# Kernel optimization log

Hardware: AMD Instinct MI355X
Metric: run time of the kernel (lower is better)

Reference implementation:

```python
import jax, jax.numpy as jnp
import numpy as np

# env_params constants (chosen, see shape_source)
ETN, EAN = 64, 64          # entity type / attribute nums
RTN, RAN = 128, 64         # relationship type / attribute nums
ME, MR = 2048, 65536       # max entities / relationships
TES, THM, HID = 16, 256, 128
ENV = ETN + RTN + TES      # 208 = GRU input size


def _lin(key, out_d, in_d):
    k1, k2 = jax.random.split(key)
    lim = 1.0 / np.sqrt(in_d)
    W = jax.random.uniform(k1, (out_d, in_d), minval=-lim, maxval=lim, dtype=jnp.float32)
    b = jax.random.uniform(k2, (out_d,), minval=-lim, maxval=lim, dtype=jnp.float32)
    return W, b


def setup_inputs() -> dict:
    key = jax.random.key(0)
    ks = jax.random.split(key, 32)
    # entity: one-hot type in cols [0:ETN], random attributes after
    etype = jax.nn.one_hot(jax.random.randint(ks[0], (ME,), 0, ETN), ETN, dtype=jnp.float32)
    entity = jnp.concatenate([etype, jax.random.normal(ks[1], (ME, EAN), jnp.float32)], axis=1)
    rtype = jax.nn.one_hot(jax.random.randint(ks[2], (MR,), 0, RTN), RTN, dtype=jnp.float32)
    relationship = jnp.concatenate([rtype, jax.random.normal(ks[3], (MR, RAN + ME), jnp.float32)], axis=1)
    target = jax.random.normal(ks[4], (ME + EAN + MR + RAN,), jnp.float32)
    action_mask = (jax.random.uniform(ks[5], (THM,)) > 0.2).astype(jnp.float32)
    # entity encoder: 128 -> 32 -> 8 -> 1
    ew1, eb1 = _lin(ks[6], 32, ETN + EAN)
    ew2, eb2 = _lin(ks[7], 8, 32)
    ew3, eb3 = _lin(ks[8], 1, 8)
    # relationship encoder: 2240 -> 128 -> 64 -> 32 -> 8 -> 1
    rin = RTN + RAN + ME
    rw1, rb1 = _lin(ks[9], 128, rin)
    rw2, rb2 = _lin(ks[10], 64, 128)
    rw3, rb3 = _lin(ks[11], 32, 64)
    rw4, rb4 = _lin(ks[12], 8, 32)
    rw5, rb5 = _lin(ks[13], 1, 8)
    # target encoder: 67712 -> 64 -> 16
    tin = ME + EAN + MR + RAN
    tw1, tb1 = _lin(ks[14], 64, tin)
    tw2, tb2 = _lin(ks[15], TES, 64)
    # GRUCell(208, 128)
    lim = 1.0 / np.sqrt(HID)
    wih = jax.random.uniform(ks[16], (3 * HID, ENV), minval=-lim, maxval=lim, dtype=jnp.float32)
    whh = jax.random.uniform(ks[17], (3 * HID, HID), minval=-lim, maxval=lim, dtype=jnp.float32)
    bih = jax.random.uniform(ks[18], (3 * HID,), minval=-lim, maxval=lim, dtype=jnp.float32)
    bhh = jax.random.uniform(ks[19], (3 * HID,), minval=-lim, maxval=lim, dtype=jnp.float32)
    hidden = jax.random.normal(ks[20], (1, HID), jnp.float32)
    aw, ab = _lin(ks[21], THM, HID)
    return dict(entity=entity, relationship=relationship, target=target, action_mask=action_mask,
                ew1=ew1, eb1=eb1, ew2=ew2, eb2=eb2, ew3=ew3, eb3=eb3,
                rw1=rw1, rb1=rb1, rw2=rw2, rb2=rb2, rw3=rw3, rb3=rb3, rw4=rw4, rb4=rb4, rw5=rw5, rb5=rb5,
                tw1=tw1, tb1=tb1, tw2=tw2, tb2=tb2,
                wih=wih, whh=whh, bih=bih, bhh=bhh, hidden=hidden, aw=aw, ab=ab)


def _masked_group_max(onehot_mask, feat):
    # onehot_mask: [N, T] (==1 where row belongs to type t); feat: [N, 1]
    m = onehot_mask == 1.0
    vals = jnp.max(jnp.where(m, feat, -jnp.inf), axis=0)      # [T]
    return jnp.where(jnp.any(m, axis=0), vals, 0.0)            # empty group -> 0


def reference(entity, relationship, target, action_mask,
              ew1, eb1, ew2, eb2, ew3, eb3,
              rw1, rb1, rw2, rb2, rw3, rb3, rw4, rb4, rw5, rb5,
              tw1, tb1, tw2, tb2,
              wih, whh, bih, bhh, hidden, aw, ab):
    relu = jax.nn.relu
    # entity encoder -> [ME, 1]
    ef = relu(entity @ ew1.T + eb1)
    ef = relu(ef @ ew2.T + eb2)
    ef = ef @ ew3.T + eb3
    # relationship encoder -> [MR, 1]
    rf = relu(relationship @ rw1.T + rb1)
    rf = relu(rf @ rw2.T + rb2)
    rf = relu(rf @ rw3.T + rb3)
    rf = relu(rf @ rw4.T + rb4)
    rf = rf @ rw5.T + rb5
    # one-hot masked segment max over type columns
    eg = _masked_group_max(entity[:, :ETN], ef)          # [ETN]
    rg = _masked_group_max(relationship[:, :RTN], rf)    # [RTN]
    # target encoder -> [TES]
    tf = relu(target @ tw1.T + tb1) @ tw2.T + tb2
    env = jnp.concatenate([eg, rg, tf]).reshape(1, ENV)
    # GRUCell (torch gate order: r, z, n)
    gx = env @ wih.T + bih
    gh = hidden @ whh.T + bhh
    xr, xz, xn = jnp.split(gx, 3, axis=1)
    hr, hz, hn = jnp.split(gh, 3, axis=1)
    r = jax.nn.sigmoid(xr + hr)
    z = jax.nn.sigmoid(xz + hz)
    n = jnp.tanh(xn + r * hn)
    h = ((1.0 - z) * n + z * hidden).reshape(-1)         # [128]
    logits = jax.nn.softmax(h @ aw.T + ab, axis=0)       # [THM]
    return logits * action_mask
```

## Files before the change

### kernel.cpp

```cpp
#include <hip/hip_runtime.h>
#include <stdint.h>

typedef unsigned short u16;
typedef short s16x8 __attribute__((ext_vector_type(8)));
typedef float f32x4 __attribute__((ext_vector_type(4)));

__device__ __forceinline__ float bf2f(u16 u) {
  union { unsigned u; float f; } c; c.u = ((unsigned)u) << 16; return c.f;
}
__device__ __forceinline__ u16 f2bf(float f) {
  union { float f; unsigned u; } c; c.f = f;
  unsigned r = c.u + 0x7FFFu + ((c.u >> 16) & 1u);
  return (u16)(r >> 16);
}
__device__ __forceinline__ unsigned encf(float x) {
  union { float f; unsigned u; } c; c.f = x;
  return (c.u & 0x80000000u) ? ~c.u : (c.u | 0x80000000u);
}
__device__ __forceinline__ float decf(unsigned e) {
  union { unsigned u; float f; } c;
  c.u = (e & 0x80000000u) ? (e ^ 0x80000000u) : ~e;
  return c.f;
}
__device__ __forceinline__ f32x4 mfma16(s16x8 a, s16x8 b, f32x4 c) {
  return __builtin_amdgcn_mfma_f32_16x16x32_bf16(a, b, c, 0, 0, 0);
}
__device__ __forceinline__ float relu(float x) { return x > 0.f ? x : 0.f; }

template <int F32>
__device__ __forceinline__ void loadf8(const void* p, size_t ei, float* o) {
  if (F32) {
    const float* f = (const float*)p + ei;
    f32x4 a = *(const f32x4*)f;
    f32x4 b = *(const f32x4*)(f + 4);
#pragma unroll
    for (int j = 0; j < 4; ++j) { o[j] = a[j]; o[4 + j] = b[j]; }
  } else {
    s16x8 v = *(const s16x8*)((const u16*)p + ei);
#pragma unroll
    for (int j = 0; j < 8; ++j) o[j] = bf2f((u16)v[j]);
  }
}
template <int F32>
__device__ __forceinline__ s16x8 load8b(const void* p, size_t ei) {
  if (F32) {
    float o[8]; loadf8<1>(p, ei, o);
    s16x8 r;
#pragma unroll
    for (int j = 0; j < 8; ++j) r[j] = (short)f2bf(o[j]);
    return r;
  } else {
    return *(const s16x8*)((const u16*)p + ei);
  }
}
template <int F32>
__device__ __forceinline__ float ld1(const void* p, size_t ei) {
  return F32 ? ((const float*)p)[ei] : bf2f(((const u16*)p)[ei]);
}

__global__ void k_detect(const u16* __restrict__ entity, const u16* __restrict__ rel,
                         unsigned* __restrict__ ws) {
  __shared__ unsigned cnt[256];
  const int t = threadIdx.x;
  ws[t] = 0u;
  unsigned c = 0;
  for (int i = t; i < 16384; i += 256) {
    unsigned u = rel[i];
    if ((u & 0x7F80u) == 0x7F80u) ++c;
  }
  for (int i = t; i < 8192; i += 256) {
    unsigned u = entity[i];
    if ((u & 0x7F80u) == 0x7F80u) ++c;
  }
  cnt[t] = c;
  __syncthreads();
  for (int st = 128; st > 0; st >>= 1) {
    if (t < st) cnt[t] += cnt[t + st];
    __syncthreads();
  }
  if (t == 0) ws[256] = cnt[0] ? 1u : 0u;
}

template <int F32>
__global__ __launch_bounds__(256) void k_ent(
    const void* __restrict__ entity, const void* __restrict__ ew1, const void* __restrict__ eb1,
    const void* __restrict__ ew2, const void* __restrict__ eb2,
    const void* __restrict__ ew3, const void* __restrict__ eb3,
    unsigned* __restrict__ egws, const unsigned* __restrict__ flag) {
  if (*flag != (unsigned)F32) return;
  __shared__ __align__(16) u16 xl[32 * 136];
  __shared__ __align__(16) u16 w1l[32 * 136];
  __shared__ float h1l[32 * 33];
  __shared__ float h2l[32 * 9];
  const int t = threadIdx.x;
  const int row0 = blockIdx.x * 32;
#pragma unroll
  for (int p = 0; p < 2; ++p) {
    int lin = p * 256 + t, rr = lin >> 4, cc = lin & 15;
    *(s16x8*)(xl + rr * 136 + cc * 8) =
        load8b<F32>(entity, (size_t)(row0 + rr) * 128 + cc * 8);
    *(s16x8*)(w1l + rr * 136 + cc * 8) = load8b<F32>(ew1, (size_t)rr * 128 + cc * 8);
  }
  __syncthreads();
  {
    const int r = t >> 3, g = t & 7;
    float acc[4] = {0.f, 0.f, 0.f, 0.f};
#pragma unroll 4
    for (int c = 0; c < 16; ++c) {
      s16x8 xv = *(const s16x8*)(xl + r * 136 + c * 8);
      float xf[8];
#pragma unroll
      for (int j = 0; j < 8; ++j) xf[j] = bf2f((u16)xv[j]);
#pragma unroll
      for (int s = 0; s < 4; ++s) {
        s16x8 wv = *(const s16x8*)(w1l + (g + 8 * s) * 136 + c * 8);
#pragma unroll
        for (int j = 0; j < 8; ++j) acc[s] += xf[j] * bf2f((u16)wv[j]);
      }
    }
#pragma unroll
    for (int s = 0; s < 4; ++s)
      h1l[r * 33 + g + 8 * s] = relu(acc[s] + ld1<F32>(eb1, g + 8 * s));
  }
  __syncthreads();
  {
    const int r = t >> 3, o = t & 7;
    float a = ld1<F32>(eb2, o);
#pragma unroll 8
    for (int k = 0; k < 32; ++k) a += h1l[r * 33 + k] * ld1<F32>(ew2, o * 32 + k);
    h2l[r * 9 + o] = relu(a);
  }
  __syncthreads();
  if (t < 32) {
    float s = ld1<F32>(eb3, 0);
#pragma unroll
    for (int k = 0; k < 8; ++k) s += h2l[t * 9 + k] * ld1<F32>(ew3, k);
    int ty = 0;
#pragma unroll
    for (int c = 0; c < 8; ++c) {
      s16x8 v = *(const s16x8*)(xl + t * 136 + c * 8);
#pragma unroll
      for (int j = 0; j < 8; ++j)
        if ((u16)v[j] == (u16)0x3F80) ty = c * 8 + j;
    }
    atomicMax(egws + ty, encf(s));
  }
}

template <int F32>
__global__ __launch_bounds__(256) void k_tgt(const void* __restrict__ target,
                                             const void* __restrict__ tw1,
                                             float* __restrict__ tpart,
                                             const unsigned* __restrict__ flag) {
  if (*flag != (unsigned)F32) return;
  __shared__ float red[256];
  const int t = threadIdx.x;
  const int o = blockIdx.x >> 2, c = blockIdx.x & 3;
  float a = 0.f;
  for (int i = t; i < 2116; i += 256) {
    float xf[8], wf[8];
    loadf8<F32>(target, (size_t)c * 16928 + i * 8, xf);
    loadf8<F32>(tw1, (size_t)o * 67712 + c * 16928 + i * 8, wf);
#pragma unroll
    for (int j = 0; j < 8; ++j) a += xf[j] * wf[j];
  }
  red[t] = a;
  __syncthreads();
  for (int st = 128; st > 0; st >>= 1) {
    if (t < st) red[t] += red[t + st];
    __syncthreads();
  }
  if (t == 0) atomicAdd(tpart + o, red[0]);
}

#define RK 2240
template <int F32>
__global__ __launch_bounds__(256) void k_rel(
    const void* __restrict__ rel, const void* __restrict__ rw1, const void* __restrict__ rb1,
    const void* __restrict__ rw2, const void* __restrict__ rb2,
    const void* __restrict__ rw3, const void* __restrict__ rb3,
    const void* __restrict__ rw4, const void* __restrict__ rb4,
    const void* __restrict__ rw5, const void* __restrict__ rb5,
    unsigned* __restrict__ rgws, const unsigned* __restrict__ flag) {
  if (*flag != (unsigned)F32) return;
  __shared__ __align__(16) unsigned char sm[53760];
  u16* smA = (u16*)sm;
  u16* smB = (u16*)(sm + 8192);
  u16* r0 = (u16*)sm;
  u16* smRF = (u16*)(sm + 18432);
  int* styp = (int*)(sm + 53248);

  const int t = threadIdx.x;
  const int lane = t & 63;
  const int wid = t >> 6;
  const int row0 = blockIdx.x * 128;
  const int fr = lane & 15, fq = lane >> 4;

  if (t < 128) {
    int ty = 0;
#pragma unroll 4
    for (int c = 0; c < 16; ++c) {
      s16x8 v = load8b<F32>(rel, (size_t)(row0 + t) * RK + c * 8);
#pragma unroll
      for (int j = 0; j < 8; ++j)
        if ((u16)v[j] == (u16)0x3F80) ty = c * 8 + j;
    }
    styp[t] = ty;
  }

  const int wm = wid >> 1, wn = wid & 1;
  f32x4 acc[4][4];
#pragma unroll
  for (int i = 0; i < 4; ++i)
#pragma unroll
    for (int j = 0; j < 4; ++j) acc[i][j] = f32x4{0.f, 0.f, 0.f, 0.f};

  const size_t gA0 = (size_t)(row0 + (t >> 2)) * RK + (t & 3) * 8;
  const size_t gB0 = (size_t)(t >> 2) * RK + (t & 3) * 8;

  for (int ki = 0; ki < 70; ++ki) {
    const int k0 = ki * 32;
    s16x8 va0 = load8b<F32>(rel, gA0 + k0);
    s16x8 va1 = load8b<F32>(rel, gA0 + (size_t)64 * RK + k0);
    s16x8 vb0 = load8b<F32>(rw1, gB0 + k0);
    s16x8 vb1 = load8b<F32>(rw1, gB0 + (size_t)64 * RK + k0);
    __syncthreads();
    *(s16x8*)(smA + t * 8) = va0;
    *(s16x8*)(smA + 2048 + t * 8) = va1;
    *(s16x8*)(smB + t * 8) = vb0;
    *(s16x8*)(smB + 2048 + t * 8) = vb1;
    __syncthreads();
    s16x8 a[4], b[4];
#pragma unroll
    for (int i = 0; i < 4; ++i)
      a[i] = *(const s16x8*)(smA + (wm * 64 + i * 16 + fr) * 32 + fq * 8);
#pragma unroll
    for (int j = 0; j < 4; ++j)
      b[j] = *(const s16x8*)(smB + (wn * 64 + j * 16 + fr) * 32 + fq * 8);
#pragma unroll
    for (int i = 0; i < 4; ++i)
#pragma unroll
      for (int j = 0; j < 4; ++j) acc[i][j] = mfma16(a[i], b[j], acc[i][j]);
  }
  __syncthreads();

#pragma unroll
  for (int j = 0; j < 4; ++j) {
    const int col = wn * 64 + j * 16 + fr;
    const float bias = ld1<F32>(rb1, col);
#pragma unroll
    for (int i = 0; i < 4; ++i) {
      const int rbase = wm * 64 + i * 16 + fq * 4;
#pragma unroll
      for (int r = 0; r < 4; ++r)
        smRF[(rbase + r) * 136 + col] = f2bf(relu(acc[i][j][r] + bias));
    }
  }
  __syncthreads();

  if (t < 128) {
    const u16* rfrow = smRF + t * 136;
    for (int o = 0; o < 64; ++o) {
      float a = ld1<F32>(rb2, o);
      for (int k = 0; k < 128; k += 8) {
        float wf[8];
        loadf8<F32>(rw2, o * 128 + k, wf);
#pragma unroll
        for (int j = 0; j < 8; ++j) a += bf2f(rfrow[k + j]) * wf[j];
      }
      r0[t * 72 + o] = f2bf(relu(a));
    }
    const u16* h2row = r0 + t * 72;
    float h3[32];
#pragma unroll
    for (int o = 0; o < 32; ++o) {
      float a = ld1<F32>(rb3, o);
      for (int k = 0; k < 64; k += 8) {
        float wf[8];
        loadf8<F32>(rw3, o * 64 + k, wf);
#pragma unroll
        for (int j = 0; j < 8; ++j) a += bf2f(h2row[k + j]) * wf[j];
      }
      h3[o] = relu(a);
    }
    float h4[8];
#pragma unroll
    for (int o = 0; o < 8; ++o) {
      float a = ld1<F32>(rb4, o);
#pragma unroll
      for (int k = 0; k < 32; ++k) a += h3[k] * ld1<F32>(rw4, o * 32 + k);
      h4[o] = relu(a);
    }
    float s = ld1<F32>(rb5, 0);
#pragma unroll
    for (int k = 0; k < 8; ++k) s += h4[k] * ld1<F32>(rw5, k);
    atomicMax(rgws + styp[t], encf(s));
  }
}

template <int F32>
__global__ __launch_bounds__(256) void k_fin(
    const unsigned* __restrict__ egws, const unsigned* __restrict__ rgws,
    const float* __restrict__ tpart, const void* __restrict__ tb1,
    const void* __restrict__ tw2, const void* __restrict__ tb2,
    const void* __restrict__ wih, const void* __restrict__ whh,
    const void* __restrict__ bih, const void* __restrict__ bhh,
    const void* __restrict__ hidden, const void* __restrict__ aw,
    const void* __restrict__ ab, const void* __restrict__ amask,
    void* __restrict__ outp, const unsigned* __restrict__ flag) {
  if (*flag != (unsigned)F32) return;
  __shared__ float env[208];
  __shared__ float th1[64];
  __shared__ float gx[384], gh[384];
  __shared__ float hv[128], hid[128];
  __shared__ float red[256];
  const int t = threadIdx.x;
  if (t < 64) {
    unsigned e = egws[t];
    env[t] = e ? decf(e) : 0.f;
    th1[t] = relu(tpart[t] + ld1<F32>(tb1, t));
  }
  if (t >= 64 && t < 192) {
    unsigned e = rgws[t - 64];
    env[t] = e ? decf(e) : 0.f;
  }
  if (t < 128) hid[t] = ld1<F32>(hidden, t);
  __syncthreads();
  if (t < 16) {
    float a = ld1<F32>(tb2, t);
    for (int k = 0; k < 64; k += 8) {
      float wf[8];
      loadf8<F32>(tw2, t * 64 + k, wf);
#pragma unroll
      for (int j = 0; j < 8; ++j) a += th1[k + j] * wf[j];
    }
    env[192 + t] = a;
  }
  __syncthreads();
  for (int o = t; o < 384; o += 256) {
    float ax = ld1<F32>(bih, o);
#pragma unroll 2
    for (int c = 0; c < 26; ++c) {
      float wf[8];
      loadf8<F32>(wih, (size_t)o * 208 + c * 8, wf);
#pragma unroll
      for (int j = 0; j < 8; ++j) ax += env[c * 8 + j] * wf[j];
    }
    gx[o] = ax;
    float ah = ld1<F32>(bhh, o);
#pragma unroll 2
    for (int c = 0; c < 16; ++c) {
      float wf[8];
      loadf8<F32>(whh, (size_t)o * 128 + c * 8, wf);
#pragma unroll
      for (int j = 0; j < 8; ++j) ah += hid[c * 8 + j] * wf[j];
    }
    gh[o] = ah;
  }
  __syncthreads();
  if (t < 128) {
    float r = 1.f / (1.f + expf(-(gx[t] + gh[t])));
    float z = 1.f / (1.f + expf(-(gx[128 + t] + gh[128 + t])));
    float n = tanhf(gx[256 + t] + r * gh[256 + t]);
    hv[t] = (1.f - z) * n + z * hid[t];
  }
  __syncthreads();
  float s = ld1<F32>(ab, t);
#pragma unroll 4
  for (int c = 0; c < 16; ++c) {
    float wf[8];
    loadf8<F32>(aw, (size_t)t * 128 + c * 8, wf);
#pragma unroll
    for (int j = 0; j < 8; ++j) s += hv[c * 8 + j] * wf[j];
  }
  red[t] = s;
  __syncthreads();
  for (int st = 128; st > 0; st >>= 1) {
    if (t < st) red[t] = fmaxf(red[t], red[t + st]);
    __syncthreads();
  }
  float m = red[0];
  __syncthreads();
  float e = expf(s - m);
  red[t] = e;
  __syncthreads();
  for (int st = 128; st > 0; st >>= 1) {
    if (t < st) red[t] += red[t + st];
    __syncthreads();
  }
  float v = e * (1.f / red[0]) * ld1<F32>(amask, t);
  if (F32) ((float*)outp)[t] = v;
  else ((u16*)outp)[t] = f2bf(v);
}

extern "C" void kernel_launch(void* const* d_in, const int* in_sizes, int n_in,
                              void* d_out, int out_size, void* d_ws, size_t ws_size,
                              hipStream_t stream) {
  const void* entity = d_in[0];
  const void* rel    = d_in[1];
  const void* target = d_in[2];
  const void* amask  = d_in[3];
  const void* ew1 = d_in[4];  const void* eb1 = d_in[5];
  const void* ew2 = d_in[6];  const void* eb2 = d_in[7];
  const void* ew3 = d_in[8];  const void* eb3 = d_in[9];
  const void* rw1 = d_in[10]; const void* rb1 = d_in[11];
  const void* rw2 = d_in[12]; const void* rb2 = d_in[13];
  const void* rw3 = d_in[14]; const void* rb3 = d_in[15];
  const void* rw4 = d_in[16]; const void* rb4 = d_in[17];
  const void* rw5 = d_in[18]; const void* rb5 = d_in[19];
  const void* tw1 = d_in[20]; const void* tb1 = d_in[21];
  const void* tw2 = d_in[22]; const void* tb2 = d_in[23];
  const void* wih = d_in[24]; const void* whh = d_in[25];
  const void* bih = d_in[26]; const void* bhh = d_in[27];
  const void* hidden = d_in[28];
  const void* aw = d_in[29];  const void* ab = d_in[30];

  unsigned* ws = (unsigned*)d_ws;
  unsigned* egws = ws;
  unsigned* rgws = ws + 64;
  float* tpart = (float*)(ws + 192);
  const unsigned* flag = ws + 256;

  hipLaunchKernelGGL(k_detect, dim3(1), dim3(256), 0, stream,
                     (const u16*)entity, (const u16*)rel, ws);

  hipLaunchKernelGGL((k_ent<0>), dim3(64), dim3(256), 0, stream,
                     entity, ew1, eb1, ew2, eb2, ew3, eb3, egws, flag);
  hipLaunchKernelGGL((k_ent<1>), dim3(64), dim3(256), 0, stream,
                     entity, ew1, eb1, ew2, eb2, ew3, eb3, egws, flag);

  hipLaunchKernelGGL((k_tgt<0>), dim3(256), dim3(256), 0, stream, target, tw1, tpart, flag);
  hipLaunchKernelGGL((k_tgt<1>), dim3(256), dim3(256), 0, stream, target, tw1, tpart, flag);

  hipLaunchKernelGGL((k_rel<0>), dim3(512), dim3(256), 0, stream,
                     rel, rw1, rb1, rw2, rb2, rw3, rb3, rw4, rb4, rw5, rb5, rgws, flag);
  hipLaunchKernelGGL((k_rel<1>), dim3(512), dim3(256), 0, stream,
                     rel, rw1, rb1, rw2, rb2, rw3, rb3, rw4, rb4, rw5, rb5, rgws, flag);

  hipLaunchKernelGGL((k_fin<0>), dim3(1), dim3(256), 0, stream,
                     egws, rgws, tpart, tb1, tw2, tb2, wih, whh, bih, bhh,
                     hidden, aw, ab, amask, d_out, flag);
  hipLaunchKernelGGL((k_fin<1>), dim3(1), dim3(256), 0, stream,
                     egws, rgws, tpart, tb1, tw2, tb2, wih, whh, bih, bhh,
                     hidden, aw, ab, amask, d_out, flag);
}
```

Measured before the change: 1.090 ms.

## Add bf16 relationship encoder kernel with async global-to-LDS double buffering

Replaces the bf16 path of the relationship encoder with a new kernel. It streams relationship rows and the first-layer weights straight into swizzled LDS using global_load_lds, double-buffered across K steps. The first two layers run on MFMA from shared memory, and the type index is found from the one-hot columns during the first K tiles. The aim is to hide global load latency and avoid register staging in the 2240-wide first layer. The cost is a large LDS footprint (about 69 KB per block), which caps occupancy.

```diff
diff --git a/kernel.cpp b/kernel.cpp
--- a/kernel.cpp
+++ b/kernel.cpp
@@ -26,6 +26,14 @@
   return __builtin_amdgcn_mfma_f32_16x16x32_bf16(a, b, c, 0, 0, 0);
 }
 __device__ __forceinline__ float relu(float x) { return x > 0.f ? x : 0.f; }
+
+__device__ __forceinline__ void gload_lds16(const void* g, void* l) {
+  auto* gp = reinterpret_cast<const __attribute__((address_space(1))) unsigned*>(
+      reinterpret_cast<uintptr_t>(g));
+  auto* lp = reinterpret_cast<__attribute__((address_space(3))) unsigned*>(
+      reinterpret_cast<uintptr_t>(l));
+  __builtin_amdgcn_global_load_lds(gp, lp, 16, 0, 0);
+}
 
 template <int F32>
 __device__ __forceinline__ void loadf8(const void* p, size_t ei, float* o) {
@@ -296,6 +304,187 @@
     for (int k = 0; k < 8; ++k) s += h4[k] * ld1<F32>(rw5, k);
     atomicMax(rgws + styp[t], encf(s));
   }
+}
+
+__global__ __launch_bounds__(256, 2) void k_relb(
+    const u16* __restrict__ rel, const u16* __restrict__ rw1, const u16* __restrict__ rb1,
+    const u16* __restrict__ rw2, const u16* __restrict__ rb2,
+    const u16* __restrict__ rw3, const u16* __restrict__ rb3,
+    const u16* __restrict__ rw4, const u16* __restrict__ rb4,
+    const u16* __restrict__ rw5, const u16* __restrict__ rb5,
+    unsigned* __restrict__ rgws, const unsigned* __restrict__ flag) {
+  if (*flag != 0u) return;
+  __shared__ __align__(16) unsigned char sm[70656];
+  const int t = threadIdx.x;
+  const int lane = t & 63;
+  const int wid = t >> 6;
+  const int fr = lane & 15, fq = lane >> 4;
+  const int wm = wid >> 1, wn = wid & 1;
+  const int l8 = lane >> 3;
+  const int row0 = blockIdx.x * 128;
+  const int swu = ((lane & 7) ^ l8) * 8;
+  const int swa = (fr & 7) << 3;
+
+  f32x4 acc[4][4];
+#pragma unroll
+  for (int i = 0; i < 4; ++i)
+#pragma unroll
+    for (int j = 0; j < 4; ++j) acc[i][j] = f32x4{0.f, 0.f, 0.f, 0.f};
+
+  {
+    unsigned char* ba = sm;
+    unsigned char* bb = sm + 16384;
+#pragma unroll
+    for (int it = 0; it < 4; ++it) {
+      const int rr = wid * 32 + it * 8;
+      gload_lds16(rel + (size_t)(row0 + rr + l8) * RK + swu, ba + rr * 128);
+      gload_lds16(rw1 + (size_t)(rr + l8) * RK + swu, bb + rr * 128);
+    }
+  }
+  __syncthreads();
+
+  int ty = 0;
+#pragma unroll 1
+  for (int ki = 0; ki < 35; ++ki) {
+    if (ki < 34) {
+      unsigned char* ba = sm + ((ki + 1) & 1) * 32768;
+      unsigned char* bb = ba + 16384;
+      const int k0 = (ki + 1) * 64;
+#pragma unroll
+      for (int it = 0; it < 4; ++it) {
+        const int rr = wid * 32 + it * 8;
+        gload_lds16(rel + (size_t)(row0 + rr + l8) * RK + k0 + swu, ba + rr * 128);
+        gload_lds16(rw1 + (size_t)(rr + l8) * RK + k0 + swu, bb + rr * 128);
+      }
+    }
+    const u16* ba = (const u16*)(sm + (ki & 1) * 32768);
+    const u16* bb = ba + 8192;
+#pragma unroll
+    for (int ks = 0; ks < 2; ++ks) {
+      s16x8 a[4], b[4];
+#pragma unroll
+      for (int i = 0; i < 4; ++i)
+        a[i] = *(const s16x8*)(ba + (wm * 64 + i * 16 + fr) * 64 + ((ks * 32 + fq * 8) ^ swa));
+#pragma unroll
+      for (int j = 0; j < 4; ++j)
+        b[j] = *(const s16x8*)(bb + (wn * 64 + j * 16 + fr) * 64 + ((ks * 32 + fq * 8) ^ swa));
+#pragma unroll
+      for (int i = 0; i < 4; ++i)
+#pragma unroll
+        for (int j = 0; j < 4; ++j) acc[i][j] = mfma16(a[i], b[j], acc[i][j]);
+    }
+    if (ki < 2) {
+      const int r = t >> 1, hs = t & 1;
+      const int rsw = (r & 7) << 3;
+#pragma unroll
+      for (int c = 0; c < 4; ++c) {
+        const int cc = hs * 4 + c;
+        s16x8 v = *(const s16x8*)(ba + r * 64 + ((cc * 8) ^ rsw));
+#pragma unroll
+        for (int j = 0; j < 8; ++j)
+          if ((u16)v[j] == (u16)0x3F80) ty = ki * 64 + cc * 8 + j;
+      }
+    }
+    __syncthreads();
+  }
+
+  u16* smRF = (u16*)sm;
+  u16* w2l = (u16*)(sm + 34816);
+  u16* h2 = (u16*)(sm + 52224);
+#pragma unroll
+  for (int j = 0; j < 4; ++j) {
+    const int col = wn * 64 + j * 16 + fr;
+    const float bias = bf2f(rb1[col]);
+#pragma unroll
+    for (int i = 0; i < 4; ++i) {
+      const int rbase = wm * 64 + i * 16 + fq * 4;
+#pragma unroll
+      for (int r = 0; r < 4; ++r)
+        smRF[(rbase + r) * 136 + col] = f2bf(relu(acc[i][j][r] + bias));
+    }
+  }
+  for (int q = t; q < 1024; q += 256) {
+    const int rr = q >> 4, cc = q & 15;
+    *(s16x8*)(w2l + rr * 136 + cc * 8) = *(const s16x8*)(rw2 + rr * 128 + cc * 8);
+  }
+  __syncthreads();
+
+  f32x4 c2[4][2];
+#pragma unroll
+  for (int i = 0; i < 4; ++i)
+#pragma unroll
+    for (int j = 0; j < 2; ++j) c2[i][j] = f32x4{0.f, 0.f, 0.f, 0.f};
+#pragma unroll
+  for (int ks = 0; ks < 4; ++ks) {
+    s16x8 a2[4], b2[2];
+#pragma unroll
+    for (int i = 0; i < 4; ++i)
+      a2[i] = *(const s16x8*)(smRF + (wm * 64 + i * 16 + fr) * 136 + ks * 32 + fq * 8);
+#pragma unroll
+    for (int j = 0; j < 2; ++j)
+      b2[j] = *(const s16x8*)(w2l + (wn * 32 + j * 16 + fr) * 136 + ks * 32 + fq * 8);
+#pragma unroll
+    for (int i = 0; i < 4; ++i)
+#pragma unroll
+      for (int j = 0; j < 2; ++j) c2[i][j] = mfma16(a2[i], b2[j], c2[i][j]);
+  }
+#pragma unroll
+  for (int j = 0; j < 2; ++j) {
+    const int col = wn * 32 + j * 16 + fr;
+    const float b2v = bf2f(rb2[col]);
+#pragma unroll
+    for (int i = 0; i < 4; ++i) {
+      const int rbase = wm * 64 + i * 16 + fq * 4;
+#pragma unroll
+      for (int r = 0; r < 4; ++r)
+        h2[(rbase + r) * 72 + col] = f2bf(relu(c2[i][j][r] + b2v));
+    }
+  }
+  __syncthreads();
+
+  const int r3 = t >> 1, hs = t & 1;
+  const u16* h2row = h2 + r3 * 72;
+  float h3a[16];
+#pragma unroll
+  for (int o = 0; o < 16; ++o) h3a[o] = bf2f(rb3[hs * 16 + o]);
+#pragma unroll 2
+  for (int kc = 0; kc < 8; ++kc) {
+    s16x8 hv = *(const s16x8*)(h2row + kc * 8);
+    float hf[8];
+#pragma unroll
+    for (int j = 0; j < 8; ++j) hf[j] = bf2f((u16)hv[j]);
+#pragma unroll
+    for (int o = 0; o < 16; ++o) {
+      s16x8 wv = *(const s16x8*)(rw3 + (size_t)(hs * 16 + o) * 64 + kc * 8);
+#pragma unroll
+      for (int j = 0; j < 8; ++j) h3a[o] += hf[j] * bf2f((u16)wv[j]);
+    }
+  }
+  float vo[16], vp[16];
+#pragma unroll
+  for (int o = 0; o < 16; ++o) {
+    vo[o] = relu(h3a[o]);
+    vp[o] = __shfl_xor(vo[o], 1);
+  }
+  float h4[4];
+#pragma unroll
+  for (int oo = 0; oo < 4; ++oo) {
+    const int o = hs * 4 + oo;
+    float s1 = 0.f, s2 = 0.f;
+#pragma unroll
+    for (int k = 0; k < 16; ++k) {
+      s1 += vo[k] * bf2f(rw4[o * 32 + hs * 16 + k]);
+      s2 += vp[k] * bf2f(rw4[o * 32 + (1 - hs) * 16 + k]);
+    }
+    h4[oo] = relu(s1 + s2 + bf2f(rb4[o]));
+  }
+  float sp = 0.f;
+#pragma unroll
+  for (int oo = 0; oo < 4; ++oo) sp += h4[oo] * bf2f(rw5[hs * 4 + oo]);
+  const float sfull = sp + __shfl_xor(sp, 1) + bf2f(rb5[0]);
+  const int tp2 = __shfl_xor(ty, 1);
+  const int tmax = ty > tp2 ? ty : tp2;
+  if (hs == 0) atomicMax(rgws + tmax, encf(sfull));
 }
 
 template <int F32>
@@ -432,8 +621,11 @@
   hipLaunchKernelGGL((k_tgt<0>), dim3(256), dim3(256), 0, stream, target, tw1, tpart, flag);
   hipLaunchKernelGGL((k_tgt<1>), dim3(256), dim3(256), 0, stream, target, tw1, tpart, flag);
 
-  hipLaunchKernelGGL((k_rel<0>), dim3(512), dim3(256), 0, stream,
-                     rel, rw1, rb1, rw2, rb2, rw3, rb3, rw4, rb4, rw5, rb5, rgws, flag);
+  hipLaunchKernelGGL(k_relb, dim3(512), dim3(256), 0, stream,
+                     (const u16*)rel, (const u16*)rw1, (const u16*)rb1,
+                     (const u16*)rw2, (const u16*)rb2, (const u16*)rw3,
+                     (const u16*)rb3, (const u16*)rw4, (const u16*)rb4,
+                     (const u16*)rw5, (const u16*)rb5, rgws, flag);
   hipLaunchKernelGGL((k_rel<1>), dim3(512), dim3(256), 0, stream,
                      rel, rw1, rb1, rw2, rb2, rw3, rb3, rw4, rb4, rw5, rb5, rgws, flag);
 
```

Result: no change. 1.086 ms (-0.4%).

## Add fp32-specialized relationship encoder kernel loading MFMA fragments from global memory

Applied to the files above, without the earlier changes.

Adds a dedicated fp32 path for the relationship encoder. It reads the fp32 rows and rw1 weights straight from global memory into registers, converts them to bf16 in registers and feeds MFMA, with no shared-memory staging of the first layer's operands. The row type is found by scanning for the one-hot column first. The goal is to cut shared-memory traffic and synchronisation in the dominant 65536x2240x128 GEMM. In exchange, each block re-reads weights from global memory or cache, loads are only 32 bytes per lane without reuse, and the later layers still run on only half the threads.

```diff
diff --git a/kernel.cpp b/kernel.cpp
--- a/kernel.cpp
+++ b/kernel.cpp
@@ -295,6 +295,140 @@
 #pragma unroll
     for (int k = 0; k < 8; ++k) s += h4[k] * ld1<F32>(rw5, k);
     atomicMax(rgws + styp[t], encf(s));
+  }
+}
+
+__global__ __launch_bounds__(256, 2) void k_relf(
+    const float* __restrict__ rel, const float* __restrict__ rw1, const float* __restrict__ rb1,
+    const float* __restrict__ rw2, const float* __restrict__ rb2,
+    const float* __restrict__ rw3, const float* __restrict__ rb3,
+    const float* __restrict__ rw4, const float* __restrict__ rb4,
+    const float* __restrict__ rw5, const float* __restrict__ rb5,
+    unsigned* __restrict__ rgws, const unsigned* __restrict__ flag) {
+  if (*flag != 1u) return;
+  __shared__ __align__(16) unsigned char sm[53760];
+  u16* r0 = (u16*)sm;
+  u16* smRF = (u16*)(sm + 18432);
+
+  const int t = threadIdx.x;
+  const int lane = t & 63;
+  const int wid = t >> 6;
+  const int row0 = blockIdx.x * 128;
+  const int fr = lane & 15, fq = lane >> 4;
+  const int wm = wid >> 1, wn = wid & 1;
+
+  int ty = 0;
+  if (t < 128) {
+    const float* rrow = rel + (size_t)(row0 + t) * RK;
+#pragma unroll 8
+    for (int c = 0; c < 128; c += 4) {
+      f32x4 v = *(const f32x4*)(rrow + c);
+#pragma unroll
+      for (int j = 0; j < 4; ++j)
+        if (v[j] == 1.0f) ty = c + j;
+    }
+  }
+
+  f32x4 acc[4][4];
+#pragma unroll
+  for (int i = 0; i < 4; ++i)
+#pragma unroll
+    for (int j = 0; j < 4; ++j) acc[i][j] = f32x4{0.f, 0.f, 0.f, 0.f};
+
+  const float* pa[4];
+  const float* pb[4];
+#pragma unroll
+  for (int i = 0; i < 4; ++i) {
+    pa[i] = rel + (size_t)(row0 + wm * 64 + i * 16 + fr) * RK + fq * 8;
+    pb[i] = rw1 + (size_t)(wn * 64 + i * 16 + fr) * RK + fq * 8;
+  }
+
+#pragma unroll 2
+  for (int ki = 0; ki < 70; ++ki) {
+    f32x4 ar[4][2], br[4][2];
+#pragma unroll
+    for (int i = 0; i < 4; ++i) {
+      ar[i][0] = *(const f32x4*)pa[i];
+      ar[i][1] = *(const f32x4*)(pa[i] + 4);
+      br[i][0] = *(const f32x4*)pb[i];
+      br[i][1] = *(const f32x4*)(pb[i] + 4);
+      pa[i] += 32;
+      pb[i] += 32;
+    }
+    s16x8 af[4], bg[4];
+#pragma unroll
+    for (int i = 0; i < 4; ++i) {
+#pragma unroll
+      for (int e = 0; e < 4; ++e) {
+        af[i][e] = (short)f2bf(ar[i][0][e]);
+        af[i][4 + e] = (short)f2bf(ar[i][1][e]);
+        bg[i][e] = (short)f2bf(br[i][0][e]);
+        bg[i][4 + e] = (short)f2bf(br[i][1][e]);
+      }
+    }
+#pragma unroll
+    for (int i = 0; i < 4; ++i)
+#pragma unroll
+      for (int j = 0; j < 4; ++j) acc[i][j] = mfma16(af[i], bg[j], acc[i][j]);
+  }
+
+#pragma unroll
+  for (int j = 0; j < 4; ++j) {
+    const int col = wn * 64 + j * 16 + fr;
+    const float bias = rb1[col];
+#pragma unroll
+    for (int i = 0; i < 4; ++i) {
+      const int rbase = wm * 64 + i * 16 + fq * 4;
+#pragma unroll
+      for (int r = 0; r < 4; ++r)
+        smRF[(rbase + r) * 136 + col] = f2bf(relu(acc[i][j][r] + bias));
+    }
+  }
+  __syncthreads();
+
+  if (t < 128) {
+    const u16* rfrow = smRF + t * 136;
+    for (int o = 0; o < 64; ++o) {
+      float a = rb2[o];
+      for (int k = 0; k < 128; k += 8) {
+        f32x4 w0 = *(const f32x4*)(rw2 + o * 128 + k);
+        f32x4 w1 = *(const f32x4*)(rw2 + o * 128 + k + 4);
+#pragma unroll
+        for (int j = 0; j < 4; ++j) {
+          a += bf2f(rfrow[k + j]) * w0[j];
+          a += bf2f(rfrow[k + 4 + j]) * w1[j];
+        }
+      }
+      r0[t * 72 + o] = f2bf(relu(a));
+    }
+    const u16* h2row = r0 + t * 72;
+    float h3[32];
+#pragma unroll
+    for (int o = 0; o < 32; ++o) {
+      float a = rb3[o];
+      for (int k = 0; k < 64; k += 8) {
+        f32x4 w0 = *(const f32x4*)(rw3 + o * 64 + k);
+        f32x4 w1 = *(const f32x4*)(rw3 + o * 64 + k + 4);
+#pragma unroll
+        for (int j = 0; j < 4; ++j) {
+          a += bf2f(h2row[k + j]) * w0[j];
+          a += bf2f(h2row[k + 4 + j]) * w1[j];
+        }
+      }
+      h3[o] = relu(a);
+    }
+    float h4[8];
+#pragma unroll
+    for (int o = 0; o < 8; ++o) {
+      float a = rb4[o];
+#pragma unroll
+      for (int k = 0; k < 32; ++k) a += h3[k] * rw4[o * 32 + k];
+      h4[o] = relu(a);
+    }
+    float s = rb5[0];
+#pragma unroll
+    for (int k = 0; k < 8; ++k) s += h4[k] * rw5[k];
+    atomicMax(rgws + ty, encf(s));
   }
 }
 
@@ -434,8 +568,11 @@
 
   hipLaunchKernelGGL((k_rel<0>), dim3(512), dim3(256), 0, stream,
                      rel, rw1, rb1, rw2, rb2, rw3, rb3, rw4, rb4, rw5, rb5, rgws, flag);
-  hipLaunchKernelGGL((k_rel<1>), dim3(512), dim3(256), 0, stream,
-                     rel, rw1, rb1, rw2, rb2, rw3, rb3, rw4, rb4, rw5, rb5, rgws, flag);
+  hipLaunchKernelGGL(k_relf, dim3(512), dim3(256), 0, stream,
+                     (const float*)rel, (const float*)rw1, (const float*)rb1,
+                     (const float*)rw2, (const float*)rb2, (const float*)rw3,
+                     (const float*)rb3, (const float*)rw4, (const float*)rb4,
+                     (const float*)rw5, (const float*)rb5, rgws, flag);
 
   hipLaunchKernelGGL((k_fin<0>), dim3(1), dim3(256), 0, stream,
                      egws, rgws, tpart, tb1, tw2, tb2, wih, whh, bih, bhh,
```

After: 1.287 ms. +18.0%, slower.
